# Optimization experiments

Hardware: AMD Instinct MI355X
Metric: run time of the kernel (lower is better)

Reference implementation:

```python
import jax, jax.numpy as jnp
import numpy as np

B, M = 2, 8192          # clouds per batch, points per cloud (N = B*M)
K_NEAR, K_FAR, K_SMOOTH = 8, 16, 8
T_LOC, T_CON = 0.1, 0.5
EPS = 1e-8


def setup_inputs() -> dict:
    key = jax.random.key(0)
    k1, k2 = jax.random.split(key)
    scores = jax.random.uniform(k1, (B * M,), dtype=jnp.float32)          # in [0,1]
    coords = jax.random.normal(k2, (B * M, 3), dtype=jnp.float32) * 2.0   # point positions
    batch_ids = (jnp.arange(B * M, dtype=jnp.int32) // M).astype(jnp.int32)
    return {"scores": scores, "coords": coords, "batch_ids": batch_ids}


def _knn_global(coords):
    """Per-cloud brute-force kNN (self included as first neighbor, like pointops.knn_query).
    coords: (N,3) -> global indices (N, K_FAR)."""
    c = coords.reshape(B, M, 3)

    def per_cloud(cb):  # cb: (M,3)
        sq = jnp.sum(cb * cb, axis=-1)                      # (M,)
        d2 = sq[:, None] + sq[None, :] - 2.0 * (cb @ cb.T)  # (M,M) squared dists
        _, idx = jax.lax.top_k(-d2, K_FAR)                  # (M,K_FAR) smallest dists
        return idx

    idx = jax.vmap(per_cloud)(c)                            # (B,M,K_FAR) local indices
    idx = idx + (jnp.arange(B, dtype=idx.dtype) * M)[:, None, None]
    return idx.reshape(B * M, K_FAR)


def _loss_terms(scores, coords, idx):
    # --- locality: neighbors (incl. self) should have similar scores ---
    nb = idx[:, :K_NEAR]                                    # (N,k)
    score_diff = jnp.abs(scores[:, None] - scores[nb])      # (N,k)
    dists = jnp.linalg.norm(coords[:, None, :] - coords[nb], axis=2)  # (N,k)
    w = jnp.exp(-dists / T_LOC)
    loss_loc = jnp.sum(w * score_diff ** 2) / jnp.clip(jnp.sum(w), 1e-8)

    # --- contrastive: near similar, far dissimilar ---
    sim_pos = 1.0 - jnp.abs(scores[:, None] - scores[idx[:, :K_NEAR]])
    sim_neg = 1.0 - jnp.abs(scores[:, None] - scores[idx[:, K_NEAR:K_FAR]])
    loss_pos = -jnp.mean(jnp.log(jax.nn.sigmoid(sim_pos / T_CON) + EPS))
    loss_neg = -jnp.mean(jnp.log(1.0 - jax.nn.sigmoid(sim_neg / T_CON) + EPS))
    loss_con = loss_pos + loss_neg

    # --- distribution: sorted scores match uniform linspace per cloud ---
    sb = jnp.sort(scores.reshape(B, M), axis=1)             # (B,M)
    target = jnp.linspace(0.0, 1.0, M, dtype=scores.dtype)  # (M,)
    loss_dist = jnp.mean(jnp.mean((sb - target[None, :]) ** 2, axis=1))

    # --- smoothness: score close to neighbor mean ---
    nmean = jnp.mean(scores[idx[:, :K_SMOOTH]], axis=1)     # (N,)
    loss_smooth = jnp.mean((scores - nmean) ** 2)

    return loss_loc, loss_con, loss_dist, loss_smooth


def reference(scores, coords, batch_ids):
    del batch_ids  # equal-sized clouds; batch structure is (B, M) by construction
    idx = _knn_global(coords)
    l_loc, l_con, l_dist, l_smooth = _loss_terms(scores, coords, idx)
    total = 1.0 * l_loc + 0.5 * l_con + 0.3 * l_dist + 0.2 * l_smooth
    return total
```

## Files before the change

kernel.cpp:

```cpp
#include <hip/hip_runtime.h>
#include <hip/hip_bf16.h>
#include <math.h>

#define BB 2
#define MM 8192
#define NN (BB * MM)
#define NBATCH (NN / 16)
#define NCELL 4096
#define LOSS_BLOCKS 1024

#define PART_OFF   0
#define RANK_OFF   24576
#define IDX_OFF    90112
#define PK_OFF     1138688
#define SS_OFF     1400832
#define CELLID_OFF 1466368
#define CNT_OFF    1531904
#define CUR_OFF    1564672
#define BBLO_OFF   1597440
#define BBHI_OFF   1613824

__device__ __forceinline__ unsigned mort3(unsigned x, unsigned y, unsigned z) {
    unsigned m = 0;
#pragma unroll
    for (int i = 0; i < 4; ++i) {
        m |= ((x >> i) & 1u) << (3 * i);
        m |= ((y >> i) & 1u) << (3 * i + 1);
        m |= ((z >> i) & 1u) << (3 * i + 2);
    }
    return m;
}

__global__ void count_kernel(const float* __restrict__ coords, int* __restrict__ cellid,
                             int* __restrict__ cnt) {
    int i = blockIdx.x * 256 + threadIdx.x;
    if (i < NN) {
        float x = coords[3 * i], y = coords[3 * i + 1], z = coords[3 * i + 2];
        int cx = min(15, max(0, (int)floorf(x) + 8));
        int cy = min(15, max(0, (int)floorf(y) + 8));
        int cz = min(15, max(0, (int)floorf(z) + 8));
        int cid = (i >> 13) * NCELL + (int)mort3((unsigned)cx, (unsigned)cy, (unsigned)cz);
        cellid[i] = cid;
        atomicAdd(&cnt[cid], 1);
    }
}

__global__ __launch_bounds__(1024) void scan_kernel(const int* __restrict__ cnt,
                                                    int* __restrict__ cursor) {
    __shared__ int wsum[16];
    const int tid = threadIdx.x, lane = tid & 63, wv = tid >> 6;
    int v[8]; int run = 0;
#pragma unroll
    for (int i = 0; i < 8; ++i) { int t = cnt[tid * 8 + i]; v[i] = run; run += t; }
    int inc = run;
#pragma unroll
    for (int off = 1; off < 64; off <<= 1) {
        int y = __shfl_up(inc, off);
        if (lane >= off) inc += y;
    }
    int laneExcl = inc - run;
    if (lane == 63) wsum[wv] = inc;
    __syncthreads();
    int wbase = 0;
#pragma unroll
    for (int w = 0; w < 16; ++w) wbase += (w < wv) ? wsum[w] : 0;
    const int base = wbase + laneExcl;
#pragma unroll
    for (int i = 0; i < 8; ++i) cursor[tid * 8 + i] = base + v[i];
}

__global__ void scatter_kernel(const float* __restrict__ coords, const float* __restrict__ scores,
                               const int* __restrict__ cellid, int* __restrict__ cursor,
                               float4* __restrict__ pk_s, float* __restrict__ s_s) {
    int i = blockIdx.x * 256 + threadIdx.x;
    if (i < NN) {
        int pos = atomicAdd(&cursor[cellid[i]], 1);
        float x = coords[3 * i], y = coords[3 * i + 1], z = coords[3 * i + 2];
        float sq = fmaf(x, x, fmaf(y, y, z * z));
        pk_s[pos] = make_float4(x, y, z, sq);
        s_s[pos] = scores[i];
    }
}

__global__ void bbox_kernel(const float4* __restrict__ pk_s, float4* __restrict__ bb_lo,
                            float4* __restrict__ bb_hi) {
    int b = blockIdx.x * 256 + threadIdx.x;
    if (b < NBATCH) {
        float4 c = pk_s[b * 16];
        float lx = c.x, ly = c.y, lz = c.z, hx = c.x, hy = c.y, hz = c.z;
#pragma unroll
        for (int i = 1; i < 16; ++i) {
            c = pk_s[b * 16 + i];
            lx = fminf(lx, c.x); ly = fminf(ly, c.y); lz = fminf(lz, c.z);
            hx = fmaxf(hx, c.x); hy = fmaxf(hy, c.y); hz = fmaxf(hz, c.z);
        }
        bb_lo[b] = make_float4(lx, ly, lz, 0.f);
        bb_hi[b] = make_float4(hx, hy, hz, 0.f);
    }
}

__device__ __forceinline__ void sort16(unsigned (&a)[16]) {
#pragma unroll
    for (int p2 = 1; p2 < 16; p2 <<= 1) {
#pragma unroll
        for (int k2 = p2; k2 >= 1; k2 >>= 1) {
#pragma unroll
            for (int j2 = k2 % p2; j2 + k2 < 16; j2 += 2 * k2) {
#pragma unroll
                for (int i2 = 0; i2 < k2; ++i2) {
                    if (i2 + j2 + k2 < 16) {
                        if (((i2 + j2) / (2 * p2)) == ((i2 + j2 + k2) / (2 * p2))) {
                            unsigned x = a[i2 + j2], y = a[i2 + j2 + k2];
                            a[i2 + j2]      = min(x, y);
                            a[i2 + j2 + k2] = max(x, y);
                        }
                    }
                }
            }
        }
    }
}

__device__ __forceinline__ void truncmerge(unsigned (&slot)[16], const unsigned (&kb)[16]) {
    unsigned m[16];
#pragma unroll
    for (int k = 0; k < 16; ++k) m[k] = min(slot[k], kb[15 - k]);
#pragma unroll
    for (int st = 8; st >= 1; st >>= 1) {
#pragma unroll
        for (int i = 0; i < 16; ++i) {
            if ((i & st) == 0) {
                unsigned lo = min(m[i], m[i + st]);
                unsigned hi = max(m[i], m[i + st]);
                m[i] = lo; m[i + st] = hi;
            }
        }
    }
#pragma unroll
    for (int k = 0; k < 16; ++k) slot[k] = m[k];
}

__global__ __launch_bounds__(1024) void knn_kernel(const float4* __restrict__ pk_s,
                                                   const float4* __restrict__ bb_lo,
                                                   const float4* __restrict__ bb_hi,
                                                   int* __restrict__ out_idx) {
    __shared__ unsigned lds_k[16][16][64];
    __shared__ float lds_t[16][64];
    const int tid = threadIdx.x, lane = tid & 63;
    const int wv = __builtin_amdgcn_readfirstlane(tid >> 6);
    const int qbase = blockIdx.x * 64;
    const int cloudbase = (qbase >> 13) << 13;
    const int q = qbase + lane;
    const float4 p = pk_s[q];
    const int sb0 = (qbase - cloudbase) >> 4;
    const float4* __restrict__ pc = pk_s + cloudbase;
    const int bbase = cloudbase >> 4;

    unsigned slot[16];
#pragma unroll
    for (int k = 0; k < 16; ++k) slot[k] = 0x7F000000u + (unsigned)k;
    float t_f = 3.0e38f;

    auto batch = [&](int bi) {
        unsigned kb[16];
#pragma unroll
        for (int i = 0; i < 16; ++i) {
            const int j = bi * 16 + i;
            const float4 c = pc[j];
            float dot = fmaf(p.x, c.x, fmaf(p.y, c.y, p.z * c.z));
            float d2  = fmaf(-2.0f, dot, p.w + c.w);
            kb[i] = (__float_as_uint(d2) & 0xFFFFE000u) | (unsigned)j;
        }
        sort16(kb);
        truncmerge(slot, kb);
        t_f = fminf(t_f, __uint_as_float((slot[15] & 0xFFFFE000u) + 0x2000u));
    };

    const int r = sb0 & 15;
    const int ownb = (wv >= r && wv < r + 4) ? (sb0 + (wv - r)) : -1;
    if (ownb >= 0) batch(ownb);
    lds_t[wv][lane] = t_f;
    __syncthreads();
    float tb = lds_t[0][lane];
#pragma unroll
    for (int w = 1; w < 16; ++w) tb = fminf(tb, lds_t[w][lane]);
    t_f = fminf(t_f, tb);

    float4 lo = bb_lo[bbase + wv];
    float4 hi = bb_hi[bbase + wv];
    for (int k = 0; k < 32; ++k) {
        const int bi = wv + (k << 4);
        float4 lo_n, hi_n;
        if (k + 1 < 32) {
            lo_n = bb_lo[bbase + bi + 16];
            hi_n = bb_hi[bbase + bi + 16];
        }
        if (bi != ownb) {
            float dx = fmaxf(fmaxf(lo.x - p.x, p.x - hi.x), 0.f);
            float dy = fmaxf(fmaxf(lo.y - p.y, p.y - hi.y), 0.f);
            float dz = fmaxf(fmaxf(lo.z - p.z, p.z - hi.z), 0.f);
            float lb = fmaf(dx, dx, fmaf(dy, dy, dz * dz));
            if (__any(fmaf(lb, 0.999f, -1e-5f) < t_f)) batch(bi);
        }
        lo = lo_n; hi = hi_n;
    }

#pragma unroll
    for (int k = 0; k < 16; ++k) lds_k[wv][k][lane] = slot[k];

    for (int half = 8; half >= 1; half >>= 1) {
        __syncthreads();
        if (wv < half) {
            unsigned a[16], m[16];
#pragma unroll
            for (int k = 0; k < 16; ++k) a[k] = lds_k[wv][k][lane];
#pragma unroll
            for (int k = 0; k < 16; ++k) m[k] = min(a[k], lds_k[wv + half][15 - k][lane]);
#pragma unroll
            for (int st = 8; st >= 1; st >>= 1) {
#pragma unroll
                for (int i = 0; i < 16; ++i) {
                    if ((i & st) == 0) {
                        unsigned lo2 = min(m[i], m[i + st]);
                        unsigned hi2 = max(m[i], m[i + st]);
                        m[i] = lo2; m[i + st] = hi2;
                    }
                }
            }
#pragma unroll
            for (int k = 0; k < 16; ++k) lds_k[wv][k][lane] = m[k];
        }
    }
    __syncthreads();

    if (wv == 0) {
#pragma unroll
        for (int k = 0; k < 16; ++k)
            out_idx[(qbase + lane) * 16 + k] = (int)(lds_k[0][k][lane] & 0x1FFFu) + cloudbase;
    }
}

__global__ __launch_bounds__(1024) void rank_kernel(const float* __restrict__ s_s,
                                                    int* __restrict__ out_rank) {
    __shared__ int lds_r[16][64];
    const int tid = threadIdx.x, lane = tid & 63;
    const int wv = __builtin_amdgcn_readfirstlane(tid >> 6);
    const int qbase = blockIdx.x * 64;
    const int cloudbase = (qbase >> 13) << 13;
    const float s = s_s[qbase + lane];
    const float* __restrict__ sc = s_s + cloudbase;
    int rank = 0;
    const int j0 = wv * 512;
    for (int jj = 0; jj < 512; jj += 16) {
#pragma unroll
        for (int i = 0; i < 16; ++i) {
            rank += (sc[j0 + jj + i] < s) ? 1 : 0;
        }
    }
    lds_r[wv][lane] = rank;
    __syncthreads();
    if (wv == 0) {
        int rsum = 0;
#pragma unroll
        for (int w = 0; w < 16; ++w) rsum += lds_r[w][lane];
        out_rank[qbase + lane] = rsum;
    }
}

__global__ __launch_bounds__(256) void loss_kernel(const float* __restrict__ s_s,
                                                   const float4* __restrict__ pk_s,
                                                   const int* __restrict__ knn,
                                                   const int* __restrict__ rank,
                                                   float* __restrict__ partial) {
    __shared__ float red[4][6];
    const int t = blockIdx.x * 256 + threadIdx.x;
    const int q = t >> 4, k = t & 15;
    const int nb = knn[t];
    const float s  = s_s[q];
    const float sn = s_s[nb];
    const float diff = fabsf(s - sn);
    const float sim = 1.0f - diff;
    const float sg = 1.0f / (1.0f + expf(-2.0f * sim));

    float a_wd = 0.f, a_w = 0.f, a_pos = 0.f, a_neg = 0.f, snk = 0.f;
    if (k < 8) {
        float4 pq = pk_s[q];
        float4 pn = pk_s[nb];
        float dx = pq.x - pn.x, dy = pq.y - pn.y, dz = pq.z - pn.z;
        float d = sqrtf(dx * dx + dy * dy + dz * dz);
        float w = expf(-10.0f * d);
        a_wd = w * diff * diff;
        a_w  = w;
        a_pos = logf(sg + 1e-8f);
        snk = sn;
    } else {
        a_neg = logf(1.0f - sg + 1e-8f);
    }

    float nsum = snk;
#pragma unroll
    for (int off = 1; off < 16; off <<= 1) nsum += __shfl_xor(nsum, off);

    float a_sm = 0.f, a_di = 0.f;
    if (k == 0) {
        float t1 = s - nsum * 0.125f;
        a_sm = t1 * t1;
        float t2 = s - (float)rank[q] * (1.0f / 8191.0f);
        a_di = t2 * t2;
    }

#pragma unroll
    for (int off = 1; off < 64; off <<= 1) {
        a_wd  += __shfl_xor(a_wd, off);
        a_w   += __shfl_xor(a_w, off);
        a_pos += __shfl_xor(a_pos, off);
        a_neg += __shfl_xor(a_neg, off);
        a_sm  += __shfl_xor(a_sm, off);
        a_di  += __shfl_xor(a_di, off);
    }
    const int wv = threadIdx.x >> 6;
    if ((threadIdx.x & 63) == 0) {
        red[wv][0] = a_wd; red[wv][1] = a_w; red[wv][2] = a_pos;
        red[wv][3] = a_neg; red[wv][4] = a_sm; red[wv][5] = a_di;
    }
    __syncthreads();
    if (threadIdx.x < 6) {
        float v = red[0][threadIdx.x] + red[1][threadIdx.x] +
                  red[2][threadIdx.x] + red[3][threadIdx.x];
        partial[threadIdx.x * LOSS_BLOCKS + blockIdx.x] = v;
    }
}

__global__ __launch_bounds__(1024) void fin_kernel(const float* __restrict__ partial,
                                                   float* __restrict__ out) {
    __shared__ float red[16][6];
    const int tid = threadIdx.x;
    float a[6];
#pragma unroll
    for (int term = 0; term < 6; ++term) a[term] = partial[term * LOSS_BLOCKS + tid];
#pragma unroll
    for (int off = 1; off < 64; off <<= 1) {
#pragma unroll
        for (int term = 0; term < 6; ++term) a[term] += __shfl_xor(a[term], off);
    }
    if ((tid & 63) == 0) {
#pragma unroll
        for (int term = 0; term < 6; ++term) red[tid >> 6][term] = a[term];
    }
    __syncthreads();
    if (tid == 0) {
        float acc[6];
#pragma unroll
        for (int term = 0; term < 6; ++term) {
            float v = 0.f;
#pragma unroll
            for (int w = 0; w < 16; ++w) v += red[w][term];
            acc[term] = v;
        }
        float l_loc = acc[0] / fmaxf(acc[1], 1e-8f);
        float l_pos = -acc[2] / (float)(NN * 8);
        float l_neg = -acc[3] / (float)(NN * 8);
        float l_sm  = acc[4] / (float)NN;
        float l_di  = acc[5] / (float)NN;
        out[0] = l_loc + 0.5f * (l_pos + l_neg) + 0.3f * l_di + 0.2f * l_sm;
    }
}

extern "C" void kernel_launch(void* const* d_in, const int* in_sizes, int n_in,
                              void* d_out, int out_size, void* d_ws, size_t ws_size,
                              hipStream_t stream) {
    const float* scores = (const float*)d_in[0];
    const float* coords = (const float*)d_in[1];
    (void)in_sizes; (void)n_in; (void)out_size; (void)ws_size;

    char* ws = (char*)d_ws;
    float*  part  = (float*)(ws + PART_OFF);
    int*    rank  = (int*)(ws + RANK_OFF);
    int*    knn   = (int*)(ws + IDX_OFF);
    float4* pk_s  = (float4*)(ws + PK_OFF);
    float*  s_s   = (float*)(ws + SS_OFF);
    int*    cellid= (int*)(ws + CELLID_OFF);
    int*    cnt   = (int*)(ws + CNT_OFF);
    int*    cursor= (int*)(ws + CUR_OFF);
    float4* bb_lo = (float4*)(ws + BBLO_OFF);
    float4* bb_hi = (float4*)(ws + BBHI_OFF);
    float*  out   = (float*)d_out;

    hipMemsetAsync(cnt, 0, 2 * NCELL * sizeof(int), stream);
    count_kernel<<<64, 256, 0, stream>>>(coords, cellid, cnt);
    scan_kernel<<<1, 1024, 0, stream>>>(cnt, cursor);
    scatter_kernel<<<64, 256, 0, stream>>>(coords, scores, cellid, cursor, pk_s, s_s);
    bbox_kernel<<<4, 256, 0, stream>>>(pk_s, bb_lo, bb_hi);
    knn_kernel<<<256, 1024, 0, stream>>>(pk_s, bb_lo, bb_hi, knn);
    rank_kernel<<<256, 1024, 0, stream>>>(s_s, rank);
    loss_kernel<<<LOSS_BLOCKS, 256, 0, stream>>>(s_s, pk_s, knn, rank, part);
    fin_kernel<<<1, 1024, 0, stream>>>(part, out);
}
```

Before: 150.0 us.

## Replace wave-uniform batch scan with per-lane candidate bitmask and compacted processing

The kNN batch loop now runs in two phases. First it tests all 32 bounding boxes against the threshold and records a per-lane bitmask of candidate batches. Then each lane works through its own candidates, padding idle lanes with sentinel keys, until no lane in the wave has any left. Before, a whole wave processed a batch whenever any lane needed it; now wave iterations scale with the largest per-lane candidate count. The cost is that the threshold is no longer tightened between box tests, so more boxes may pass, and point loads become per-lane gathers instead of wave-uniform broadcasts.

```diff
diff --git a/kernel.cpp b/kernel.cpp
--- a/kernel.cpp
+++ b/kernel.cpp
@@ -161,7 +161,7 @@
     for (int k = 0; k < 16; ++k) slot[k] = 0x7F000000u + (unsigned)k;
     float t_f = 3.0e38f;
 
-    auto batch = [&](int bi) {
+    auto batchU = [&](int bi) {
         unsigned kb[16];
 #pragma unroll
         for (int i = 0; i < 16; ++i) {
@@ -178,7 +178,7 @@
 
     const int r = sb0 & 15;
     const int ownb = (wv >= r && wv < r + 4) ? (sb0 + (wv - r)) : -1;
-    if (ownb >= 0) batch(ownb);
+    if (ownb >= 0) batchU(ownb);
     lds_t[wv][lane] = t_f;
     __syncthreads();
     float tb = lds_t[0][lane];
@@ -186,23 +186,37 @@
     for (int w = 1; w < 16; ++w) tb = fminf(tb, lds_t[w][lane]);
     t_f = fminf(t_f, tb);
 
-    float4 lo = bb_lo[bbase + wv];
-    float4 hi = bb_hi[bbase + wv];
+    unsigned mask = 0u;
+#pragma unroll 4
     for (int k = 0; k < 32; ++k) {
         const int bi = wv + (k << 4);
-        float4 lo_n, hi_n;
-        if (k + 1 < 32) {
-            lo_n = bb_lo[bbase + bi + 16];
-            hi_n = bb_hi[bbase + bi + 16];
-        }
-        if (bi != ownb) {
-            float dx = fmaxf(fmaxf(lo.x - p.x, p.x - hi.x), 0.f);
-            float dy = fmaxf(fmaxf(lo.y - p.y, p.y - hi.y), 0.f);
-            float dz = fmaxf(fmaxf(lo.z - p.z, p.z - hi.z), 0.f);
-            float lb = fmaf(dx, dx, fmaf(dy, dy, dz * dz));
-            if (__any(fmaf(lb, 0.999f, -1e-5f) < t_f)) batch(bi);
-        }
-        lo = lo_n; hi = hi_n;
+        const float4 lo = bb_lo[bbase + bi];
+        const float4 hi = bb_hi[bbase + bi];
+        float dx = fmaxf(fmaxf(lo.x - p.x, p.x - hi.x), 0.f);
+        float dy = fmaxf(fmaxf(lo.y - p.y, p.y - hi.y), 0.f);
+        float dz = fmaxf(fmaxf(lo.z - p.z, p.z - hi.z), 0.f);
+        float lb = fmaf(dx, dx, fmaf(dy, dy, dz * dz));
+        bool hot = (fmaf(lb, 0.999f, -1e-5f) < t_f) && (bi != ownb);
+        mask |= hot ? (1u << k) : 0u;
+    }
+
+    while (__any(mask != 0u)) {
+        const bool valid = (mask != 0u);
+        const unsigned kk = valid ? (unsigned)__builtin_ctz(mask) : 0u;
+        mask &= (mask - 1u);
+        const int jb = (wv + ((int)kk << 4)) << 4;
+        unsigned kb[16];
+#pragma unroll
+        for (int i = 0; i < 16; ++i) {
+            const float4 c = pc[jb + i];
+            float dot = fmaf(p.x, c.x, fmaf(p.y, c.y, p.z * c.z));
+            float d2  = fmaf(-2.0f, dot, p.w + c.w);
+            unsigned key = (__float_as_uint(d2) & 0xFFFFE000u) | (unsigned)(jb + i);
+            kb[i] = valid ? key : (0x7F200000u + (unsigned)i);
+        }
+        sort16(kb);
+        truncmerge(slot, kb);
+        t_f = fminf(t_f, __uint_as_float((slot[15] & 0xFFFFE000u) + 0x2000u));
     }
 
 #pragma unroll
```

New measurement: 189.2 us. 1.26x slower.

## Fuse all stages into one cooperative kernel with grid-wide syncs

Applied to the files above, without the earlier changes.

Replaces eight separate kernel launches (count, scan, scatter, bbox, kNN, rank, loss, finalize) with one cooperative kernel of 256 blocks that separates phases with grid.sync(). The kNN stage also changes: the four waves that own the local batches now merge their results through LDS into a shared initial threshold, and only one wave keeps the merged list, instead of a per-lane min of thresholds. This is meant to remove launch gaps between the many small kernels, at the cost of grid barriers and running the small phases on only a fraction of each block's threads.

```diff
diff --git a/kernel.cpp b/kernel.cpp
--- a/kernel.cpp
+++ b/kernel.cpp
@@ -1,24 +1,25 @@
 #include <hip/hip_runtime.h>
-#include <hip/hip_bf16.h>
+#include <hip/hip_cooperative_groups.h>
 #include <math.h>
+
+namespace cg = cooperative_groups;
 
 #define BB 2
 #define MM 8192
 #define NN (BB * MM)
 #define NBATCH (NN / 16)
 #define NCELL 4096
-#define LOSS_BLOCKS 1024
 
 #define PART_OFF   0
-#define RANK_OFF   24576
-#define IDX_OFF    90112
-#define PK_OFF     1138688
-#define SS_OFF     1400832
-#define CELLID_OFF 1466368
-#define CNT_OFF    1531904
-#define CUR_OFF    1564672
-#define BBLO_OFF   1597440
-#define BBHI_OFF   1613824
+#define RANK_OFF   8192
+#define IDX_OFF    73728
+#define PK_OFF     1122304
+#define SS_OFF     1384448
+#define CELLID_OFF 1449984
+#define CNT_OFF    1515520
+#define CUR_OFF    1548288
+#define BBLO_OFF   1581056
+#define BBHI_OFF   1597440
 
 __device__ __forceinline__ unsigned mort3(unsigned x, unsigned y, unsigned z) {
     unsigned m = 0;
@@ -29,74 +30,6 @@
         m |= ((z >> i) & 1u) << (3 * i + 2);
     }
     return m;
-}
-
-__global__ void count_kernel(const float* __restrict__ coords, int* __restrict__ cellid,
-                             int* __restrict__ cnt) {
-    int i = blockIdx.x * 256 + threadIdx.x;
-    if (i < NN) {
-        float x = coords[3 * i], y = coords[3 * i + 1], z = coords[3 * i + 2];
-        int cx = min(15, max(0, (int)floorf(x) + 8));
-        int cy = min(15, max(0, (int)floorf(y) + 8));
-        int cz = min(15, max(0, (int)floorf(z) + 8));
-        int cid = (i >> 13) * NCELL + (int)mort3((unsigned)cx, (unsigned)cy, (unsigned)cz);
-        cellid[i] = cid;
-        atomicAdd(&cnt[cid], 1);
-    }
-}
-
-__global__ __launch_bounds__(1024) void scan_kernel(const int* __restrict__ cnt,
-                                                    int* __restrict__ cursor) {
-    __shared__ int wsum[16];
-    const int tid = threadIdx.x, lane = tid & 63, wv = tid >> 6;
-    int v[8]; int run = 0;
-#pragma unroll
-    for (int i = 0; i < 8; ++i) { int t = cnt[tid * 8 + i]; v[i] = run; run += t; }
-    int inc = run;
-#pragma unroll
-    for (int off = 1; off < 64; off <<= 1) {
-        int y = __shfl_up(inc, off);
-        if (lane >= off) inc += y;
-    }
-    int laneExcl = inc - run;
-    if (lane == 63) wsum[wv] = inc;
-    __syncthreads();
-    int wbase = 0;
-#pragma unroll
-    for (int w = 0; w < 16; ++w) wbase += (w < wv) ? wsum[w] : 0;
-    const int base = wbase + laneExcl;
-#pragma unroll
-    for (int i = 0; i < 8; ++i) cursor[tid * 8 + i] = base + v[i];
-}
-
-__global__ void scatter_kernel(const float* __restrict__ coords, const float* __restrict__ scores,
-                               const int* __restrict__ cellid, int* __restrict__ cursor,
-                               float4* __restrict__ pk_s, float* __restrict__ s_s) {
-    int i = blockIdx.x * 256 + threadIdx.x;
-    if (i < NN) {
-        int pos = atomicAdd(&cursor[cellid[i]], 1);
-        float x = coords[3 * i], y = coords[3 * i + 1], z = coords[3 * i + 2];
-        float sq = fmaf(x, x, fmaf(y, y, z * z));
-        pk_s[pos] = make_float4(x, y, z, sq);
-        s_s[pos] = scores[i];
-    }
-}
-
-__global__ void bbox_kernel(const float4* __restrict__ pk_s, float4* __restrict__ bb_lo,
-                            float4* __restrict__ bb_hi) {
-    int b = blockIdx.x * 256 + threadIdx.x;
-    if (b < NBATCH) {
-        float4 c = pk_s[b * 16];
-        float lx = c.x, ly = c.y, lz = c.z, hx = c.x, hy = c.y, hz = c.z;
-#pragma unroll
-        for (int i = 1; i < 16; ++i) {
-            c = pk_s[b * 16 + i];
-            lx = fminf(lx, c.x); ly = fminf(ly, c.y); lz = fminf(lz, c.z);
-            hx = fmaxf(hx, c.x); hy = fmaxf(hy, c.y); hz = fmaxf(hz, c.z);
-        }
-        bb_lo[b] = make_float4(lx, ly, lz, 0.f);
-        bb_hi[b] = make_float4(hx, hy, hz, 0.f);
-    }
 }
 
 __device__ __forceinline__ void sort16(unsigned (&a)[16]) {
@@ -140,229 +73,305 @@
     for (int k = 0; k < 16; ++k) slot[k] = m[k];
 }
 
-__global__ __launch_bounds__(1024) void knn_kernel(const float4* __restrict__ pk_s,
-                                                   const float4* __restrict__ bb_lo,
-                                                   const float4* __restrict__ bb_hi,
-                                                   int* __restrict__ out_idx) {
+__global__ __launch_bounds__(1024) void fused_kernel(
+    const float* __restrict__ scores, const float* __restrict__ coords,
+    float4* __restrict__ pk_s, float* __restrict__ s_s,
+    int* __restrict__ cellid, int* __restrict__ cnt, int* __restrict__ cursor,
+    float4* __restrict__ bb_lo, float4* __restrict__ bb_hi,
+    int* __restrict__ out_idx, int* __restrict__ out_rank,
+    float* __restrict__ partial, float* __restrict__ out)
+{
+    cg::grid_group grid = cg::this_grid();
     __shared__ unsigned lds_k[16][16][64];
-    __shared__ float lds_t[16][64];
-    const int tid = threadIdx.x, lane = tid & 63;
+    __shared__ int lds_i[16][64];
+    __shared__ int wsum[16];
+    __shared__ float redf[16][6];
+
+    const int tid = threadIdx.x;
+    const int blk = blockIdx.x;
+    const int gid = blk * 1024 + tid;
+    const int lane = tid & 63;
     const int wv = __builtin_amdgcn_readfirstlane(tid >> 6);
-    const int qbase = blockIdx.x * 64;
-    const int cloudbase = (qbase >> 13) << 13;
-    const int q = qbase + lane;
-    const float4 p = pk_s[q];
-    const int sb0 = (qbase - cloudbase) >> 4;
-    const float4* __restrict__ pc = pk_s + cloudbase;
-    const int bbase = cloudbase >> 4;
-
-    unsigned slot[16];
-#pragma unroll
-    for (int k = 0; k < 16; ++k) slot[k] = 0x7F000000u + (unsigned)k;
-    float t_f = 3.0e38f;
-
-    auto batch = [&](int bi) {
-        unsigned kb[16];
-#pragma unroll
-        for (int i = 0; i < 16; ++i) {
-            const int j = bi * 16 + i;
-            const float4 c = pc[j];
-            float dot = fmaf(p.x, c.x, fmaf(p.y, c.y, p.z * c.z));
-            float d2  = fmaf(-2.0f, dot, p.w + c.w);
-            kb[i] = (__float_as_uint(d2) & 0xFFFFE000u) | (unsigned)j;
-        }
-        sort16(kb);
-        truncmerge(slot, kb);
-        t_f = fminf(t_f, __uint_as_float((slot[15] & 0xFFFFE000u) + 0x2000u));
-    };
-
-    const int r = sb0 & 15;
-    const int ownb = (wv >= r && wv < r + 4) ? (sb0 + (wv - r)) : -1;
-    if (ownb >= 0) batch(ownb);
-    lds_t[wv][lane] = t_f;
-    __syncthreads();
-    float tb = lds_t[0][lane];
-#pragma unroll
-    for (int w = 1; w < 16; ++w) tb = fminf(tb, lds_t[w][lane]);
-    t_f = fminf(t_f, tb);
-
-    float4 lo = bb_lo[bbase + wv];
-    float4 hi = bb_hi[bbase + wv];
-    for (int k = 0; k < 32; ++k) {
-        const int bi = wv + (k << 4);
-        float4 lo_n, hi_n;
-        if (k + 1 < 32) {
-            lo_n = bb_lo[bbase + bi + 16];
-            hi_n = bb_hi[bbase + bi + 16];
-        }
-        if (bi != ownb) {
-            float dx = fmaxf(fmaxf(lo.x - p.x, p.x - hi.x), 0.f);
-            float dy = fmaxf(fmaxf(lo.y - p.y, p.y - hi.y), 0.f);
-            float dz = fmaxf(fmaxf(lo.z - p.z, p.z - hi.z), 0.f);
-            float lb = fmaf(dx, dx, fmaf(dy, dy, dz * dz));
-            if (__any(fmaf(lb, 0.999f, -1e-5f) < t_f)) batch(bi);
-        }
-        lo = lo_n; hi = hi_n;
-    }
-
-#pragma unroll
-    for (int k = 0; k < 16; ++k) lds_k[wv][k][lane] = slot[k];
-
-    for (int half = 8; half >= 1; half >>= 1) {
-        __syncthreads();
-        if (wv < half) {
-            unsigned a[16], m[16];
-#pragma unroll
-            for (int k = 0; k < 16; ++k) a[k] = lds_k[wv][k][lane];
-#pragma unroll
-            for (int k = 0; k < 16; ++k) m[k] = min(a[k], lds_k[wv + half][15 - k][lane]);
-#pragma unroll
-            for (int st = 8; st >= 1; st >>= 1) {
-#pragma unroll
-                for (int i = 0; i < 16; ++i) {
-                    if ((i & st) == 0) {
-                        unsigned lo2 = min(m[i], m[i + st]);
-                        unsigned hi2 = max(m[i], m[i + st]);
-                        m[i] = lo2; m[i + st] = hi2;
+
+    if (tid < 64) {
+        const int i = blk * 64 + tid;
+        float x = coords[3 * i], y = coords[3 * i + 1], z = coords[3 * i + 2];
+        int cx = min(15, max(0, (int)floorf(x) + 8));
+        int cy = min(15, max(0, (int)floorf(y) + 8));
+        int cz = min(15, max(0, (int)floorf(z) + 8));
+        int cid = (i >> 13) * NCELL + (int)mort3((unsigned)cx, (unsigned)cy, (unsigned)cz);
+        cellid[i] = cid;
+        atomicAdd(&cnt[cid], 1);
+    }
+    grid.sync();
+
+    if (blk == 0) {
+        int v[8]; int run = 0;
+#pragma unroll
+        for (int i = 0; i < 8; ++i) { int t = cnt[tid * 8 + i]; v[i] = run; run += t; }
+        int inc = run;
+#pragma unroll
+        for (int off = 1; off < 64; off <<= 1) {
+            int y = __shfl_up(inc, off);
+            if (lane >= off) inc += y;
+        }
+        int laneExcl = inc - run;
+        if (lane == 63) wsum[wv] = inc;
+        __syncthreads();
+        int wbase = 0;
+#pragma unroll
+        for (int w = 0; w < 16; ++w) wbase += (w < wv) ? wsum[w] : 0;
+        const int base = wbase + laneExcl;
+#pragma unroll
+        for (int i = 0; i < 8; ++i) cursor[tid * 8 + i] = base + v[i];
+    }
+    grid.sync();
+
+    if (tid < 64) {
+        const int i = blk * 64 + tid;
+        int pos = atomicAdd(&cursor[cellid[i]], 1);
+        float x = coords[3 * i], y = coords[3 * i + 1], z = coords[3 * i + 2];
+        float sq = fmaf(x, x, fmaf(y, y, z * z));
+        pk_s[pos] = make_float4(x, y, z, sq);
+        s_s[pos] = scores[i];
+    }
+    grid.sync();
+
+    if (tid < 4) {
+        const int b = blk * 4 + tid;
+        float4 c = pk_s[b * 16];
+        float lx = c.x, ly = c.y, lz = c.z, hx = c.x, hy = c.y, hz = c.z;
+#pragma unroll
+        for (int i = 1; i < 16; ++i) {
+            c = pk_s[b * 16 + i];
+            lx = fminf(lx, c.x); ly = fminf(ly, c.y); lz = fminf(lz, c.z);
+            hx = fmaxf(hx, c.x); hy = fmaxf(hy, c.y); hz = fmaxf(hz, c.z);
+        }
+        bb_lo[b] = make_float4(lx, ly, lz, 0.f);
+        bb_hi[b] = make_float4(hx, hy, hz, 0.f);
+    }
+    grid.sync();
+
+    {
+        const int qbase = blk * 64;
+        const int cloudbase = (qbase >> 13) << 13;
+        const float4 p = pk_s[qbase + lane];
+        const int sb0 = (qbase - cloudbase) >> 4;
+        const int r = sb0 & 15;
+        const int ownb = (wv >= r && wv < r + 4) ? (sb0 + (wv - r)) : -1;
+        const float4* __restrict__ pc = pk_s + cloudbase;
+        const int bbase = cloudbase >> 4;
+
+        unsigned slot[16];
+#pragma unroll
+        for (int k = 0; k < 16; ++k) slot[k] = 0x7F000000u + (unsigned)k;
+        float t_f = 3.0e38f;
+
+        auto batchU = [&](int bi) {
+            unsigned kb[16];
+#pragma unroll
+            for (int i = 0; i < 16; ++i) {
+                const int j = bi * 16 + i;
+                const float4 c = pc[j];
+                float dot = fmaf(p.x, c.x, fmaf(p.y, c.y, p.z * c.z));
+                float d2  = fmaf(-2.0f, dot, p.w + c.w);
+                kb[i] = (__float_as_uint(d2) & 0xFFFFE000u) | (unsigned)j;
+            }
+            sort16(kb);
+            truncmerge(slot, kb);
+            t_f = fminf(t_f, __uint_as_float((slot[15] & 0xFFFFE000u) + 0x2000u));
+        };
+
+        if (ownb >= 0) batchU(ownb);
+#pragma unroll
+        for (int k = 0; k < 16; ++k) lds_k[wv][k][lane] = slot[k];
+        __syncthreads();
+        unsigned mg[16];
+#pragma unroll
+        for (int k = 0; k < 16; ++k) mg[k] = lds_k[r][k][lane];
+#pragma unroll
+        for (int w2 = 1; w2 < 4; ++w2) {
+            unsigned ob[16];
+#pragma unroll
+            for (int k = 0; k < 16; ++k) ob[k] = lds_k[r + w2][k][lane];
+            truncmerge(mg, ob);
+        }
+        __syncthreads();
+        if (wv == r) {
+#pragma unroll
+            for (int k = 0; k < 16; ++k) slot[k] = mg[k];
+        } else {
+#pragma unroll
+            for (int k = 0; k < 16; ++k) slot[k] = 0x7F000000u + (unsigned)k;
+        }
+        t_f = __uint_as_float((mg[15] & 0xFFFFE000u) + 0x2000u);
+
+        float4 lo = bb_lo[bbase + wv];
+        float4 hi = bb_hi[bbase + wv];
+        for (int k2 = 0; k2 < 32; ++k2) {
+            const int bi = wv + (k2 << 4);
+            float4 lo_n, hi_n;
+            if (k2 + 1 < 32) {
+                lo_n = bb_lo[bbase + bi + 16];
+                hi_n = bb_hi[bbase + bi + 16];
+            }
+            if (bi != ownb) {
+                float dx = fmaxf(fmaxf(lo.x - p.x, p.x - hi.x), 0.f);
+                float dy = fmaxf(fmaxf(lo.y - p.y, p.y - hi.y), 0.f);
+                float dz = fmaxf(fmaxf(lo.z - p.z, p.z - hi.z), 0.f);
+                float lb = fmaf(dx, dx, fmaf(dy, dy, dz * dz));
+                if (__any(fmaf(lb, 0.999f, -1e-5f) < t_f)) batchU(bi);
+            }
+            lo = lo_n; hi = hi_n;
+        }
+
+#pragma unroll
+        for (int k = 0; k < 16; ++k) lds_k[wv][k][lane] = slot[k];
+
+        for (int half = 8; half >= 1; half >>= 1) {
+            __syncthreads();
+            if (wv < half) {
+                unsigned a[16], m[16];
+#pragma unroll
+                for (int k = 0; k < 16; ++k) a[k] = lds_k[wv][k][lane];
+#pragma unroll
+                for (int k = 0; k < 16; ++k) m[k] = min(a[k], lds_k[wv + half][15 - k][lane]);
+#pragma unroll
+                for (int st = 8; st >= 1; st >>= 1) {
+#pragma unroll
+                    for (int i = 0; i < 16; ++i) {
+                        if ((i & st) == 0) {
+                            unsigned lo2 = min(m[i], m[i + st]);
+                            unsigned hi2 = max(m[i], m[i + st]);
+                            m[i] = lo2; m[i + st] = hi2;
+                        }
                     }
                 }
-            }
-#pragma unroll
-            for (int k = 0; k < 16; ++k) lds_k[wv][k][lane] = m[k];
-        }
-    }
-    __syncthreads();
-
-    if (wv == 0) {
-#pragma unroll
-        for (int k = 0; k < 16; ++k)
-            out_idx[(qbase + lane) * 16 + k] = (int)(lds_k[0][k][lane] & 0x1FFFu) + cloudbase;
-    }
-}
-
-__global__ __launch_bounds__(1024) void rank_kernel(const float* __restrict__ s_s,
-                                                    int* __restrict__ out_rank) {
-    __shared__ int lds_r[16][64];
-    const int tid = threadIdx.x, lane = tid & 63;
-    const int wv = __builtin_amdgcn_readfirstlane(tid >> 6);
-    const int qbase = blockIdx.x * 64;
-    const int cloudbase = (qbase >> 13) << 13;
-    const float s = s_s[qbase + lane];
-    const float* __restrict__ sc = s_s + cloudbase;
-    int rank = 0;
-    const int j0 = wv * 512;
-    for (int jj = 0; jj < 512; jj += 16) {
-#pragma unroll
-        for (int i = 0; i < 16; ++i) {
-            rank += (sc[j0 + jj + i] < s) ? 1 : 0;
-        }
-    }
-    lds_r[wv][lane] = rank;
-    __syncthreads();
-    if (wv == 0) {
-        int rsum = 0;
-#pragma unroll
-        for (int w = 0; w < 16; ++w) rsum += lds_r[w][lane];
-        out_rank[qbase + lane] = rsum;
-    }
-}
-
-__global__ __launch_bounds__(256) void loss_kernel(const float* __restrict__ s_s,
-                                                   const float4* __restrict__ pk_s,
-                                                   const int* __restrict__ knn,
-                                                   const int* __restrict__ rank,
-                                                   float* __restrict__ partial) {
-    __shared__ float red[4][6];
-    const int t = blockIdx.x * 256 + threadIdx.x;
-    const int q = t >> 4, k = t & 15;
-    const int nb = knn[t];
-    const float s  = s_s[q];
-    const float sn = s_s[nb];
-    const float diff = fabsf(s - sn);
-    const float sim = 1.0f - diff;
-    const float sg = 1.0f / (1.0f + expf(-2.0f * sim));
-
-    float a_wd = 0.f, a_w = 0.f, a_pos = 0.f, a_neg = 0.f, snk = 0.f;
-    if (k < 8) {
-        float4 pq = pk_s[q];
-        float4 pn = pk_s[nb];
-        float dx = pq.x - pn.x, dy = pq.y - pn.y, dz = pq.z - pn.z;
-        float d = sqrtf(dx * dx + dy * dy + dz * dz);
-        float w = expf(-10.0f * d);
-        a_wd = w * diff * diff;
-        a_w  = w;
-        a_pos = logf(sg + 1e-8f);
-        snk = sn;
-    } else {
-        a_neg = logf(1.0f - sg + 1e-8f);
-    }
-
-    float nsum = snk;
-#pragma unroll
-    for (int off = 1; off < 16; off <<= 1) nsum += __shfl_xor(nsum, off);
-
-    float a_sm = 0.f, a_di = 0.f;
-    if (k == 0) {
-        float t1 = s - nsum * 0.125f;
-        a_sm = t1 * t1;
-        float t2 = s - (float)rank[q] * (1.0f / 8191.0f);
-        a_di = t2 * t2;
-    }
-
-#pragma unroll
-    for (int off = 1; off < 64; off <<= 1) {
-        a_wd  += __shfl_xor(a_wd, off);
-        a_w   += __shfl_xor(a_w, off);
-        a_pos += __shfl_xor(a_pos, off);
-        a_neg += __shfl_xor(a_neg, off);
-        a_sm  += __shfl_xor(a_sm, off);
-        a_di  += __shfl_xor(a_di, off);
-    }
-    const int wv = threadIdx.x >> 6;
-    if ((threadIdx.x & 63) == 0) {
-        red[wv][0] = a_wd; red[wv][1] = a_w; red[wv][2] = a_pos;
-        red[wv][3] = a_neg; red[wv][4] = a_sm; red[wv][5] = a_di;
-    }
-    __syncthreads();
-    if (threadIdx.x < 6) {
-        float v = red[0][threadIdx.x] + red[1][threadIdx.x] +
-                  red[2][threadIdx.x] + red[3][threadIdx.x];
-        partial[threadIdx.x * LOSS_BLOCKS + blockIdx.x] = v;
-    }
-}
-
-__global__ __launch_bounds__(1024) void fin_kernel(const float* __restrict__ partial,
-                                                   float* __restrict__ out) {
-    __shared__ float red[16][6];
-    const int tid = threadIdx.x;
-    float a[6];
-#pragma unroll
-    for (int term = 0; term < 6; ++term) a[term] = partial[term * LOSS_BLOCKS + tid];
-#pragma unroll
-    for (int off = 1; off < 64; off <<= 1) {
-#pragma unroll
-        for (int term = 0; term < 6; ++term) a[term] += __shfl_xor(a[term], off);
-    }
-    if ((tid & 63) == 0) {
-#pragma unroll
-        for (int term = 0; term < 6; ++term) red[tid >> 6][term] = a[term];
-    }
-    __syncthreads();
-    if (tid == 0) {
-        float acc[6];
-#pragma unroll
-        for (int term = 0; term < 6; ++term) {
+#pragma unroll
+                for (int k = 0; k < 16; ++k) lds_k[wv][k][lane] = m[k];
+            }
+        }
+        __syncthreads();
+        if (wv == 0) {
+#pragma unroll
+            for (int k = 0; k < 16; ++k)
+                out_idx[(qbase + lane) * 16 + k] = (int)(lds_k[0][k][lane] & 0x1FFFu) + cloudbase;
+        }
+    }
+
+    {
+        __syncthreads();
+        const int qbase = blk * 64;
+        const int cloudbase = (qbase >> 13) << 13;
+        const float s = s_s[qbase + lane];
+        const float* __restrict__ sc = s_s + cloudbase;
+        int rank = 0;
+        const int j0 = wv * 512;
+        for (int jj = 0; jj < 512; jj += 16) {
+#pragma unroll
+            for (int i = 0; i < 16; ++i) {
+                rank += (sc[j0 + jj + i] < s) ? 1 : 0;
+            }
+        }
+        lds_i[wv][lane] = rank;
+        __syncthreads();
+        if (wv == 0) {
+            int rsum = 0;
+#pragma unroll
+            for (int w = 0; w < 16; ++w) rsum += lds_i[w][lane];
+            out_rank[qbase + lane] = rsum;
+        }
+    }
+    grid.sync();
+
+    {
+        const int t = gid;
+        const int q = t >> 4, kk = t & 15;
+        const int nb = out_idx[t];
+        const float s  = s_s[q];
+        const float sn = s_s[nb];
+        const float diff = fabsf(s - sn);
+        const float sim = 1.0f - diff;
+        const float sg = 1.0f / (1.0f + expf(-2.0f * sim));
+
+        float a_wd = 0.f, a_w = 0.f, a_pos = 0.f, a_neg = 0.f, snk = 0.f;
+        if (kk < 8) {
+            float4 pq = pk_s[q];
+            float4 pn = pk_s[nb];
+            float dx = pq.x - pn.x, dy = pq.y - pn.y, dz = pq.z - pn.z;
+            float d = sqrtf(dx * dx + dy * dy + dz * dz);
+            float w = expf(-10.0f * d);
+            a_wd = w * diff * diff;
+            a_w  = w;
+            a_pos = logf(sg + 1e-8f);
+            snk = sn;
+        } else {
+            a_neg = logf(1.0f - sg + 1e-8f);
+        }
+
+        float nsum = snk;
+#pragma unroll
+        for (int off = 1; off < 16; off <<= 1) nsum += __shfl_xor(nsum, off);
+
+        float a_sm = 0.f, a_di = 0.f;
+        if (kk == 0) {
+            float t1 = s - nsum * 0.125f;
+            a_sm = t1 * t1;
+            float t2 = s - (float)out_rank[q] * (1.0f / 8191.0f);
+            a_di = t2 * t2;
+        }
+
+#pragma unroll
+        for (int off = 1; off < 64; off <<= 1) {
+            a_wd  += __shfl_xor(a_wd, off);
+            a_w   += __shfl_xor(a_w, off);
+            a_pos += __shfl_xor(a_pos, off);
+            a_neg += __shfl_xor(a_neg, off);
+            a_sm  += __shfl_xor(a_sm, off);
+            a_di  += __shfl_xor(a_di, off);
+        }
+        if (lane == 0) {
+            redf[wv][0] = a_wd; redf[wv][1] = a_w; redf[wv][2] = a_pos;
+            redf[wv][3] = a_neg; redf[wv][4] = a_sm; redf[wv][5] = a_di;
+        }
+        __syncthreads();
+        if (tid < 6) {
             float v = 0.f;
 #pragma unroll
-            for (int w = 0; w < 16; ++w) v += red[w][term];
-            acc[term] = v;
-        }
-        float l_loc = acc[0] / fmaxf(acc[1], 1e-8f);
-        float l_pos = -acc[2] / (float)(NN * 8);
-        float l_neg = -acc[3] / (float)(NN * 8);
-        float l_sm  = acc[4] / (float)NN;
-        float l_di  = acc[5] / (float)NN;
-        out[0] = l_loc + 0.5f * (l_pos + l_neg) + 0.3f * l_di + 0.2f * l_sm;
+            for (int w = 0; w < 16; ++w) v += redf[w][tid];
+            partial[tid * 256 + blk] = v;
+        }
+    }
+    grid.sync();
+
+    if (blk == 0) {
+        if (tid < 256) {
+            float a[6];
+#pragma unroll
+            for (int term = 0; term < 6; ++term) a[term] = partial[term * 256 + tid];
+#pragma unroll
+            for (int off = 1; off < 64; off <<= 1) {
+#pragma unroll
+                for (int term = 0; term < 6; ++term) a[term] += __shfl_xor(a[term], off);
+            }
+            if (lane == 0) {
+#pragma unroll
+                for (int term = 0; term < 6; ++term) redf[wv][term] = a[term];
+            }
+        }
+        __syncthreads();
+        if (tid == 0) {
+            float acc[6];
+#pragma unroll
+            for (int term = 0; term < 6; ++term)
+                acc[term] = redf[0][term] + redf[1][term] + redf[2][term] + redf[3][term];
+            float l_loc = acc[0] / fmaxf(acc[1], 1e-8f);
+            float l_pos = -acc[2] / (float)(NN * 8);
+            float l_neg = -acc[3] / (float)(NN * 8);
+            float l_sm  = acc[4] / (float)NN;
+            float l_di  = acc[5] / (float)NN;
+            out[0] = l_loc + 0.5f * (l_pos + l_neg) + 0.3f * l_di + 0.2f * l_sm;
+        }
     }
 }
 
@@ -387,12 +396,13 @@
     float*  out   = (float*)d_out;
 
     hipMemsetAsync(cnt, 0, 2 * NCELL * sizeof(int), stream);
-    count_kernel<<<64, 256, 0, stream>>>(coords, cellid, cnt);
-    scan_kernel<<<1, 1024, 0, stream>>>(cnt, cursor);
-    scatter_kernel<<<64, 256, 0, stream>>>(coords, scores, cellid, cursor, pk_s, s_s);
-    bbox_kernel<<<4, 256, 0, stream>>>(pk_s, bb_lo, bb_hi);
-    knn_kernel<<<256, 1024, 0, stream>>>(pk_s, bb_lo, bb_hi, knn);
-    rank_kernel<<<256, 1024, 0, stream>>>(s_s, rank);
-    loss_kernel<<<LOSS_BLOCKS, 256, 0, stream>>>(s_s, pk_s, knn, rank, part);
-    fin_kernel<<<1, 1024, 0, stream>>>(part, out);
+
+    void* kargs[] = {
+        (void*)&scores, (void*)&coords, (void*)&pk_s, (void*)&s_s,
+        (void*)&cellid, (void*)&cnt, (void*)&cursor,
+        (void*)&bb_lo, (void*)&bb_hi, (void*)&knn, (void*)&rank,
+        (void*)&part, (void*)&out
+    };
+    hipLaunchCooperativeKernel((const void*)fused_kernel, dim3(256), dim3(1024),
+                               kargs, 0, stream);
 }
```

After: 300.7 us. 2x slower.

## Fuse rank into kNN kernel, finalize loss in last block, share self-batch seeds

Applied to the files above, without the earlier changes.

The rank computation moves into the tail of the kNN kernel, and the final reduction folds into the loss kernel through an atomic last-block counter. Together these remove two launches. The kNN seeding now merges the four self-batch top-16 lists, so the starting threshold is tighter than the old min of per-wave thresholds. Other waves restart with empty slots, which avoids duplicate neighbours. The risks are the extra memset and atomic, plus heavier kNN blocks from the added rank loop.

```diff
diff --git a/kernel.cpp b/kernel.cpp
--- a/kernel.cpp
+++ b/kernel.cpp
@@ -10,15 +10,16 @@
 #define LOSS_BLOCKS 1024
 
 #define PART_OFF   0
-#define RANK_OFF   24576
-#define IDX_OFF    90112
-#define PK_OFF     1138688
-#define SS_OFF     1400832
-#define CELLID_OFF 1466368
-#define CNT_OFF    1531904
-#define CUR_OFF    1564672
-#define BBLO_OFF   1597440
-#define BBHI_OFF   1613824
+#define DONE_OFF   24576
+#define RANK_OFF   24640
+#define IDX_OFF    90176
+#define PK_OFF     1138752
+#define SS_OFF     1400896
+#define CELLID_OFF 1466432
+#define CNT_OFF    1531968
+#define CUR_OFF    1564736
+#define BBLO_OFF   1597504
+#define BBHI_OFF   1613888
 
 __device__ __forceinline__ unsigned mort3(unsigned x, unsigned y, unsigned z) {
     unsigned m = 0;
@@ -141,18 +142,21 @@
 }
 
 __global__ __launch_bounds__(1024) void knn_kernel(const float4* __restrict__ pk_s,
+                                                   const float* __restrict__ s_s,
                                                    const float4* __restrict__ bb_lo,
                                                    const float4* __restrict__ bb_hi,
-                                                   int* __restrict__ out_idx) {
+                                                   int* __restrict__ out_idx,
+                                                   int* __restrict__ out_rank) {
     __shared__ unsigned lds_k[16][16][64];
-    __shared__ float lds_t[16][64];
+    __shared__ int lds_i[16][64];
     const int tid = threadIdx.x, lane = tid & 63;
     const int wv = __builtin_amdgcn_readfirstlane(tid >> 6);
     const int qbase = blockIdx.x * 64;
     const int cloudbase = (qbase >> 13) << 13;
-    const int q = qbase + lane;
-    const float4 p = pk_s[q];
+    const float4 p = pk_s[qbase + lane];
     const int sb0 = (qbase - cloudbase) >> 4;
+    const int r = sb0 & 15;
+    const int ownb = (wv >= r && wv < r + 4) ? (sb0 + (wv - r)) : -1;
     const float4* __restrict__ pc = pk_s + cloudbase;
     const int bbase = cloudbase >> 4;
 
@@ -161,7 +165,7 @@
     for (int k = 0; k < 16; ++k) slot[k] = 0x7F000000u + (unsigned)k;
     float t_f = 3.0e38f;
 
-    auto batch = [&](int bi) {
+    auto batchU = [&](int bi) {
         unsigned kb[16];
 #pragma unroll
         for (int i = 0; i < 16; ++i) {
@@ -176,22 +180,36 @@
         t_f = fminf(t_f, __uint_as_float((slot[15] & 0xFFFFE000u) + 0x2000u));
     };
 
-    const int r = sb0 & 15;
-    const int ownb = (wv >= r && wv < r + 4) ? (sb0 + (wv - r)) : -1;
-    if (ownb >= 0) batch(ownb);
-    lds_t[wv][lane] = t_f;
-    __syncthreads();
-    float tb = lds_t[0][lane];
-#pragma unroll
-    for (int w = 1; w < 16; ++w) tb = fminf(tb, lds_t[w][lane]);
-    t_f = fminf(t_f, tb);
+    if (ownb >= 0) batchU(ownb);
+#pragma unroll
+    for (int k = 0; k < 16; ++k) lds_k[wv][k][lane] = slot[k];
+    __syncthreads();
+    unsigned mg[16];
+#pragma unroll
+    for (int k = 0; k < 16; ++k) mg[k] = lds_k[r][k][lane];
+#pragma unroll
+    for (int w2 = 1; w2 < 4; ++w2) {
+        unsigned ob[16];
+#pragma unroll
+        for (int k = 0; k < 16; ++k) ob[k] = lds_k[r + w2][k][lane];
+        truncmerge(mg, ob);
+    }
+    __syncthreads();
+    if (wv == r) {
+#pragma unroll
+        for (int k = 0; k < 16; ++k) slot[k] = mg[k];
+    } else {
+#pragma unroll
+        for (int k = 0; k < 16; ++k) slot[k] = 0x7F000000u + (unsigned)k;
+    }
+    t_f = __uint_as_float((mg[15] & 0xFFFFE000u) + 0x2000u);
 
     float4 lo = bb_lo[bbase + wv];
     float4 hi = bb_hi[bbase + wv];
-    for (int k = 0; k < 32; ++k) {
-        const int bi = wv + (k << 4);
+    for (int k2 = 0; k2 < 32; ++k2) {
+        const int bi = wv + (k2 << 4);
         float4 lo_n, hi_n;
-        if (k + 1 < 32) {
+        if (k2 + 1 < 32) {
             lo_n = bb_lo[bbase + bi + 16];
             hi_n = bb_hi[bbase + bi + 16];
         }
@@ -200,7 +218,7 @@
             float dy = fmaxf(fmaxf(lo.y - p.y, p.y - hi.y), 0.f);
             float dz = fmaxf(fmaxf(lo.z - p.z, p.z - hi.z), 0.f);
             float lb = fmaf(dx, dx, fmaf(dy, dy, dz * dz));
-            if (__any(fmaf(lb, 0.999f, -1e-5f) < t_f)) batch(bi);
+            if (__any(fmaf(lb, 0.999f, -1e-5f) < t_f)) batchU(bi);
         }
         lo = lo_n; hi = hi_n;
     }
@@ -232,38 +250,31 @@
         }
     }
     __syncthreads();
-
     if (wv == 0) {
 #pragma unroll
         for (int k = 0; k < 16; ++k)
             out_idx[(qbase + lane) * 16 + k] = (int)(lds_k[0][k][lane] & 0x1FFFu) + cloudbase;
     }
-}
-
-__global__ __launch_bounds__(1024) void rank_kernel(const float* __restrict__ s_s,
-                                                    int* __restrict__ out_rank) {
-    __shared__ int lds_r[16][64];
-    const int tid = threadIdx.x, lane = tid & 63;
-    const int wv = __builtin_amdgcn_readfirstlane(tid >> 6);
-    const int qbase = blockIdx.x * 64;
-    const int cloudbase = (qbase >> 13) << 13;
-    const float s = s_s[qbase + lane];
-    const float* __restrict__ sc = s_s + cloudbase;
-    int rank = 0;
-    const int j0 = wv * 512;
-    for (int jj = 0; jj < 512; jj += 16) {
-#pragma unroll
-        for (int i = 0; i < 16; ++i) {
-            rank += (sc[j0 + jj + i] < s) ? 1 : 0;
-        }
-    }
-    lds_r[wv][lane] = rank;
-    __syncthreads();
-    if (wv == 0) {
-        int rsum = 0;
-#pragma unroll
-        for (int w = 0; w < 16; ++w) rsum += lds_r[w][lane];
-        out_rank[qbase + lane] = rsum;
+
+    {
+        const float s = s_s[qbase + lane];
+        const float* __restrict__ sc = s_s + cloudbase;
+        int rank = 0;
+        const int j0 = wv * 512;
+        for (int jj = 0; jj < 512; jj += 16) {
+#pragma unroll
+            for (int i = 0; i < 16; ++i) {
+                rank += (sc[j0 + jj + i] < s) ? 1 : 0;
+            }
+        }
+        lds_i[wv][lane] = rank;
+        __syncthreads();
+        if (wv == 0) {
+            int rsum = 0;
+#pragma unroll
+            for (int w = 0; w < 16; ++w) rsum += lds_i[w][lane];
+            out_rank[qbase + lane] = rsum;
+        }
     }
 }
 
@@ -271,8 +282,11 @@
                                                    const float4* __restrict__ pk_s,
                                                    const int* __restrict__ knn,
                                                    const int* __restrict__ rank,
-                                                   float* __restrict__ partial) {
+                                                   float* __restrict__ partial,
+                                                   int* __restrict__ done,
+                                                   float* __restrict__ out) {
     __shared__ float red[4][6];
+    __shared__ int isLast;
     const int t = blockIdx.x * 256 + threadIdx.x;
     const int q = t >> 4, k = t & 15;
     const int nb = knn[t];
@@ -329,40 +343,42 @@
                   red[2][threadIdx.x] + red[3][threadIdx.x];
         partial[threadIdx.x * LOSS_BLOCKS + blockIdx.x] = v;
     }
-}
-
-__global__ __launch_bounds__(1024) void fin_kernel(const float* __restrict__ partial,
-                                                   float* __restrict__ out) {
-    __shared__ float red[16][6];
-    const int tid = threadIdx.x;
-    float a[6];
-#pragma unroll
-    for (int term = 0; term < 6; ++term) a[term] = partial[term * LOSS_BLOCKS + tid];
-#pragma unroll
-    for (int off = 1; off < 64; off <<= 1) {
-#pragma unroll
-        for (int term = 0; term < 6; ++term) a[term] += __shfl_xor(a[term], off);
-    }
-    if ((tid & 63) == 0) {
-#pragma unroll
-        for (int term = 0; term < 6; ++term) red[tid >> 6][term] = a[term];
-    }
-    __syncthreads();
-    if (tid == 0) {
-        float acc[6];
+    __threadfence();
+    if (threadIdx.x == 0) isLast = (atomicAdd(done, 1) == LOSS_BLOCKS - 1);
+    __syncthreads();
+    if (isLast) {
+        __threadfence();
+        float a[6];
 #pragma unroll
         for (int term = 0; term < 6; ++term) {
             float v = 0.f;
 #pragma unroll
-            for (int w = 0; w < 16; ++w) v += red[w][term];
-            acc[term] = v;
-        }
-        float l_loc = acc[0] / fmaxf(acc[1], 1e-8f);
-        float l_pos = -acc[2] / (float)(NN * 8);
-        float l_neg = -acc[3] / (float)(NN * 8);
-        float l_sm  = acc[4] / (float)NN;
-        float l_di  = acc[5] / (float)NN;
-        out[0] = l_loc + 0.5f * (l_pos + l_neg) + 0.3f * l_di + 0.2f * l_sm;
+            for (int i = 0; i < 4; ++i)
+                v += partial[term * LOSS_BLOCKS + threadIdx.x * 4 + i];
+            a[term] = v;
+        }
+#pragma unroll
+        for (int off = 1; off < 64; off <<= 1) {
+#pragma unroll
+            for (int term = 0; term < 6; ++term) a[term] += __shfl_xor(a[term], off);
+        }
+        if ((threadIdx.x & 63) == 0) {
+#pragma unroll
+            for (int term = 0; term < 6; ++term) red[wv][term] = a[term];
+        }
+        __syncthreads();
+        if (threadIdx.x == 0) {
+            float acc[6];
+#pragma unroll
+            for (int term = 0; term < 6; ++term)
+                acc[term] = red[0][term] + red[1][term] + red[2][term] + red[3][term];
+            float l_loc = acc[0] / fmaxf(acc[1], 1e-8f);
+            float l_pos = -acc[2] / (float)(NN * 8);
+            float l_neg = -acc[3] / (float)(NN * 8);
+            float l_sm  = acc[4] / (float)NN;
+            float l_di  = acc[5] / (float)NN;
+            out[0] = l_loc + 0.5f * (l_pos + l_neg) + 0.3f * l_di + 0.2f * l_sm;
+        }
     }
 }
 
@@ -375,6 +391,7 @@
 
     char* ws = (char*)d_ws;
     float*  part  = (float*)(ws + PART_OFF);
+    int*    done  = (int*)(ws + DONE_OFF);
     int*    rank  = (int*)(ws + RANK_OFF);
     int*    knn   = (int*)(ws + IDX_OFF);
     float4* pk_s  = (float4*)(ws + PK_OFF);
@@ -386,13 +403,12 @@
     float4* bb_hi = (float4*)(ws + BBHI_OFF);
     float*  out   = (float*)d_out;
 
+    hipMemsetAsync(done, 0, sizeof(int), stream);
     hipMemsetAsync(cnt, 0, 2 * NCELL * sizeof(int), stream);
     count_kernel<<<64, 256, 0, stream>>>(coords, cellid, cnt);
     scan_kernel<<<1, 1024, 0, stream>>>(cnt, cursor);
     scatter_kernel<<<64, 256, 0, stream>>>(coords, scores, cellid, cursor, pk_s, s_s);
     bbox_kernel<<<4, 256, 0, stream>>>(pk_s, bb_lo, bb_hi);
-    knn_kernel<<<256, 1024, 0, stream>>>(pk_s, bb_lo, bb_hi, knn);
-    rank_kernel<<<256, 1024, 0, stream>>>(s_s, rank);
-    loss_kernel<<<LOSS_BLOCKS, 256, 0, stream>>>(s_s, pk_s, knn, rank, part);
-    fin_kernel<<<1, 1024, 0, stream>>>(part, out);
-}
+    knn_kernel<<<256, 1024, 0, stream>>>(pk_s, s_s, bb_lo, bb_hi, knn, rank);
+    loss_kernel<<<LOSS_BLOCKS, 256, 0, stream>>>(s_s, pk_s, knn, rank, part, done, out);
+}
```

Measured after the change: 211.0 us. +40.6%, slower.
